# Performance work log

Hardware: AMD Instinct MI355X
Metric: run time of the kernel (lower is better)

## Reference

```python
import jax, jax.numpy as jnp
import numpy as np

V, E, H, D = 32000, 512, 512, 512  # vocab, emb_dim, enc_hid_dim, dec_hid_dim
B, S, T = 32, 64, 48               # batch, src_len, trg_len


def _gru_cell(x, h, Wih, Whh, bih, bhh):
    # PyTorch GRU cell semantics (gate order r, z, n)
    gi = x @ Wih.T + bih
    gh = h @ Whh.T + bhh
    ir, iz, i_n = jnp.split(gi, 3, axis=-1)
    hr, hz, h_n = jnp.split(gh, 3, axis=-1)
    r = jax.nn.sigmoid(ir + hr)
    z = jax.nn.sigmoid(iz + hz)
    n = jnp.tanh(i_n + r * h_n)
    return (1.0 - z) * n + z * h


def setup_inputs() -> dict:
    key = jax.random.key(0)
    ks = jax.random.split(key, 21)
    f = lambda k, shp: jax.random.normal(k, shp, dtype=jnp.float32) * 0.05
    inp = {
        'src': jax.random.randint(ks[0], (B, S), 0, V),
        'trg': jax.random.randint(ks[1], (T, B), 0, V),
        'emb': f(ks[2], (V, E)),
        'encf_Wih': f(ks[3], (3 * H, E)), 'encf_Whh': f(ks[4], (3 * H, H)),
        'encf_bih': f(ks[5], (3 * H,)), 'encf_bhh': f(ks[6], (3 * H,)),
        'encb_Wih': f(ks[7], (3 * H, E)), 'encb_Whh': f(ks[8], (3 * H, H)),
        'encb_bih': f(ks[9], (3 * H,)), 'encb_bhh': f(ks[10], (3 * H,)),
        'fc_W': f(ks[11], (D, 2 * H)), 'fc_b': f(ks[12], (D,)),
        'attn_W': f(ks[13], (D, D + 2 * H)), 'attn_v': f(ks[14], (D,)),
        'dec_Wih': f(ks[15], (3 * D, E + 2 * H)), 'dec_Whh': f(ks[16], (3 * D, D)),
        'dec_bih': f(ks[17], (3 * D,)), 'dec_bhh': f(ks[18], (3 * D,)),
        'out_W': f(ks[19], (V, 2 * H + D + E)),
        'out_b': jnp.zeros((V,), dtype=jnp.float32),
    }
    return inp


def _forward(src, trg, emb, encf_Wih, encf_Whh, encf_bih, encf_bhh,
             encb_Wih, encb_Whh, encb_bih, encb_bhh, fc_W, fc_b,
             attn_W, attn_v, dec_Wih, dec_Whh, dec_bih, dec_bhh, out_W, out_b):
    x = emb[src]                       # [B,S,E]
    xT = jnp.swapaxes(x, 0, 1)         # [S,B,E]
    h0 = jnp.zeros((src.shape[0], encf_Whh.shape[1]), dtype=x.dtype)

    def stepf(h, xt):
        h2 = _gru_cell(xt, h, encf_Wih, encf_Whh, encf_bih, encf_bhh)
        return h2, h2

    def stepb(h, xt):
        h2 = _gru_cell(xt, h, encb_Wih, encb_Whh, encb_bih, encb_bhh)
        return h2, h2

    hf, yf = jax.lax.scan(stepf, h0, xT)
    hb, yb = jax.lax.scan(stepb, h0, xT[::-1])
    # [B,S,2H] bidirectional encoder outputs (backward stream re-reversed)
    enc_out = jnp.concatenate([jnp.swapaxes(yf, 0, 1), jnp.swapaxes(yb[::-1], 0, 1)], axis=-1)
    # decoder init state from final fwd/bwd hidden
    s0 = jnp.tanh(jnp.concatenate([hf, hb], axis=-1) @ fc_W.T + fc_b)  # [B,D]

    def dec_step(s, tok):
        e = emb[tok]  # [B,E]
        srep = jnp.broadcast_to(s[:, None, :], (s.shape[0], enc_out.shape[1], s.shape[1]))
        energy = jnp.tanh(jnp.concatenate([srep, enc_out], axis=-1) @ attn_W.T)  # [B,S,D]
        a = jax.nn.softmax(energy @ attn_v, axis=1)  # [B,S]
        c = jnp.einsum('bs,bsh->bh', a, enc_out)     # [B,2H]
        s2 = _gru_cell(jnp.concatenate([e, c], axis=-1), s, dec_Wih, dec_Whh, dec_bih, dec_bhh)
        pred = jnp.concatenate([s2, c, e], axis=-1) @ out_W.T + out_b  # [B,V]
        return s2, pred

    # teacher forcing: decoder inputs are trg[0..T-2]
    _, preds = jax.lax.scan(dec_step, s0, trg[:-1])
    out0 = jnp.zeros((1,) + preds.shape[1:], dtype=preds.dtype)  # outputs[0] stays zero
    return jnp.concatenate([out0, preds], axis=0)  # [T,B,V]


def reference(src, trg, emb, encf_Wih, encf_Whh, encf_bih, encf_bhh,
              encb_Wih, encb_Whh, encb_bih, encb_bhh, fc_W, fc_b,
              attn_W, attn_v, dec_Wih, dec_Whh, dec_bih, dec_bhh, out_W, out_b):
    return _forward(src, trg, emb, encf_Wih, encf_Whh, encf_bih, encf_bhh,
                    encb_Wih, encb_Whh, encb_bih, encb_bhh, fc_W, fc_b,
                    attn_W, attn_v, dec_Wih, dec_Whh, dec_bih, dec_bhh, out_W, out_b)
```

## Files before the change

kernel.cpp:

```cpp
#include <hip/hip_runtime.h>
#include <stdint.h>
#include <stddef.h>

typedef __attribute__((ext_vector_type(8))) short short8;
typedef __attribute__((ext_vector_type(4))) float f32x4;
typedef unsigned int u32;

__device__ inline unsigned short f2bf(float f) {
  union { float f; uint32_t u; } v; v.f = f;
  uint32_t u = v.u;
  u += 0x7FFFu + ((u >> 16) & 1u);
  return (unsigned short)(u >> 16);
}
__device__ inline float bf2f(unsigned short h) {
  union { uint32_t u; float f; } v; v.u = ((uint32_t)h) << 16; return v.f;
}
__device__ inline short8 pack8(float4 a, float4 b) {
  short8 r;
  r[0] = (short)f2bf(a.x); r[1] = (short)f2bf(a.y);
  r[2] = (short)f2bf(a.z); r[3] = (short)f2bf(a.w);
  r[4] = (short)f2bf(b.x); r[5] = (short)f2bf(b.y);
  r[6] = (short)f2bf(b.z); r[7] = (short)f2bf(b.w);
  return r;
}
__device__ inline float tanh_fast(float x) {
  float xc = fminf(fmaxf(x, -9.f), 9.f);
  float e = __expf(2.f * xc);
  return (e - 1.f) * __builtin_amdgcn_rcpf(e + 1.f);
}
__device__ inline float sigm_fast(float x) {
  float xc = fminf(fmaxf(x, -30.f), 30.f);
  return __builtin_amdgcn_rcpf(1.f + __expf(-xc));
}
__device__ inline void gl_lds16(const unsigned short* g, unsigned short* l) {
  __builtin_amdgcn_global_load_lds(
      (const __attribute__((address_space(1))) u32*)g,
      (__attribute__((address_space(3))) u32*)l, 16, 0, 0);
}

__global__ __launch_bounds__(128) void prep_gather(
    const int* __restrict__ src, const int* __restrict__ trg,
    const float* __restrict__ emb,
    unsigned short* __restrict__ xbf, unsigned short* __restrict__ ebf,
    unsigned short* __restrict__ Zbf) {
  int r = blockIdx.x, tid = threadIdx.x;
  if (r < 2048) {
    int b = r & 31, s = r >> 5;
    int tok = src[b * 64 + s];
    const float* e = emb + (size_t)tok * 512;
    float4 v = *(const float4*)(e + tid * 4);
    unsigned short* dst = xbf + (size_t)r * 512 + tid * 4;
    dst[0] = f2bf(v.x); dst[1] = f2bf(v.y); dst[2] = f2bf(v.z); dst[3] = f2bf(v.w);
  } else {
    int rr = r - 2048;
    int t = rr >> 5, b = rr & 31;
    unsigned short* dst = ebf + (size_t)rr * 512 + tid * 4;
    if (t < 47) {
      int tok = trg[t * 32 + b];
      const float* e = emb + (size_t)tok * 512;
      float4 v = *(const float4*)(e + tid * 4);
      unsigned short q0 = f2bf(v.x), q1 = f2bf(v.y), q2 = f2bf(v.z), q3 = f2bf(v.w);
      dst[0] = q0; dst[1] = q1; dst[2] = q2; dst[3] = q3;
      unsigned short* zd = Zbf + (size_t)rr * 2048 + 1536 + tid * 4;
      zd[0] = q0; zd[1] = q1; zd[2] = q2; zd[3] = q3;
    } else {
      dst[0] = 0; dst[1] = 0; dst[2] = 0; dst[3] = 0;
    }
  }
}

__global__ __launch_bounds__(64) void cvt_weights(
    const float* __restrict__ encfW, const float* __restrict__ encbW,
    const float* __restrict__ attnW, const float* __restrict__ decWhh,
    unsigned short* __restrict__ whFbf, unsigned short* __restrict__ whBbf,
    unsigned short* __restrict__ Wcat) {
  int r = blockIdx.x, c = threadIdx.x * 8;
  const float* s;
  unsigned short* d;
  if (r < 1536) { s = encfW + (size_t)r * 512 + c; d = whFbf + (size_t)r * 512 + c; }
  else if (r < 3072) { int q = r - 1536; s = encbW + (size_t)q * 512 + c; d = whBbf + (size_t)q * 512 + c; }
  else if (r < 3584) { int q = r - 3072; s = attnW + (size_t)q * 1536 + c; d = Wcat + (size_t)q * 512 + c; }
  else { int q = r - 3584; s = decWhh + (size_t)q * 512 + c; d = Wcat + (size_t)(q + 512) * 512 + c; }
  *(short8*)d = pack8(*(const float4*)s, *(const float4*)(s + 4));
}

template <bool ABF, bool BBF, bool WBF>
__global__ __launch_bounds__(256) void gemm_kernel(
    const void* __restrict__ Av, int lda,
    const void* __restrict__ Bv, int ldb, int bco,
    const float* __restrict__ bias,
    void* __restrict__ Cv, int ldc,
    int K, int Mvalid, int row_off) {
  __shared__ __align__(16) unsigned short As[128 * 32];
  __shared__ __align__(16) unsigned short Bs[128 * 32];
  const int tid = threadIdx.x;
  const int m0 = blockIdx.x * 128, n0 = blockIdx.y * 128;
  const int w = tid >> 6, lane = tid & 63;
  const int wm = w >> 1, wn = w & 1;
  const int fr = lane & 15, fq = lane >> 4;
  f32x4 acc[4][4];
#pragma unroll
  for (int mi = 0; mi < 4; ++mi)
#pragma unroll
    for (int ni = 0; ni < 4; ++ni) acc[mi][ni] = (f32x4){0.f, 0.f, 0.f, 0.f};
  for (int k0 = 0; k0 < K; k0 += 32) {
#pragma unroll
    for (int p = 0; p < 2; ++p) {
      int idx = p * 256 + tid;
      int row = idx >> 2, seg = idx & 3;
      if (ABF) {
        const unsigned short* Ab = (const unsigned short*)Av;
        *(short8*)(As + row * 32 + seg * 8) =
            *(const short8*)(Ab + (size_t)(m0 + row) * lda + k0 + seg * 8);
      } else {
        const float* Af = (const float*)Av;
        const float* ap = Af + (size_t)(m0 + row) * lda + k0 + seg * 8;
        *(short8*)(As + row * 32 + seg * 8) = pack8(*(const float4*)ap, *(const float4*)(ap + 4));
      }
      if (BBF) {
        const unsigned short* Bb = (const unsigned short*)Bv;
        *(short8*)(Bs + row * 32 + seg * 8) =
            *(const short8*)(Bb + (size_t)(n0 + row) * ldb + bco + k0 + seg * 8);
      } else {
        const float* Bf = (const float*)Bv;
        const float* bp = Bf + (size_t)(n0 + row) * ldb + bco + k0 + seg * 8;
        *(short8*)(Bs + row * 32 + seg * 8) = pack8(*(const float4*)bp, *(const float4*)(bp + 4));
      }
    }
    __syncthreads();
    short8 af[4], bfr[4];
#pragma unroll
    for (int mi = 0; mi < 4; ++mi)
      af[mi] = *(const short8*)(As + (wm * 64 + mi * 16 + fr) * 32 + fq * 8);
#pragma unroll
    for (int ni = 0; ni < 4; ++ni)
      bfr[ni] = *(const short8*)(Bs + (wn * 64 + ni * 16 + fr) * 32 + fq * 8);
#pragma unroll
    for (int mi = 0; mi < 4; ++mi)
#pragma unroll
      for (int ni = 0; ni < 4; ++ni)
        acc[mi][ni] = __builtin_amdgcn_mfma_f32_16x16x32_bf16(af[mi], bfr[ni], acc[mi][ni], 0, 0, 0);
    __syncthreads();
  }
#pragma unroll
  for (int mi = 0; mi < 4; ++mi)
#pragma unroll
    for (int ni = 0; ni < 4; ++ni) {
      int col = n0 + wn * 64 + ni * 16 + fr;
      float bv = bias ? bias[col] : 0.f;
#pragma unroll
      for (int j = 0; j < 4; ++j) {
        int rowm = m0 + wm * 64 + mi * 16 + fq * 4 + j;
        if (rowm < Mvalid) {
          float val = acc[mi][ni][j] + bv;
          if (WBF)
            ((unsigned short*)Cv)[(size_t)(rowm + row_off) * ldc + col] = f2bf(val);
          else
            ((float*)Cv)[(size_t)(rowm + row_off) * ldc + col] = val;
        }
      }
    }
}

__global__ __launch_bounds__(512, 1) void gemm_big8(
    const unsigned short* __restrict__ A,
    const unsigned short* __restrict__ B,
    const float* __restrict__ bias,
    float* __restrict__ C) {
  extern __shared__ char lds[];
  char* LA = lds;
  char* LB = lds + 65536;
  const int tid = threadIdx.x;
  const int w = tid >> 6, lane = tid & 63;
  int wg = blockIdx.x;
  {
    int x = wg & 7, i = wg >> 3;
    wg = (x < 6 ? x * 94 : 564 + (x - 6) * 93) + i;
  }
  const int m0 = (wg % 6) * 256, n0 = (wg / 6) * 256;
  const int wm = w >> 2, wn = w & 3;
  const int fr = lane & 15, fq = lane >> 4;

  auto stage = [&](const unsigned short* G, char* L, int rowbase, int kt, int h, int c) {
#pragma unroll
    for (int j = 0; j < 2; ++j) {
      int pbh = j * 8192 + w * 1024;
      int pl = pbh + lane * 16;
      int lb = pl ^ (((pl >> 7) & 7) << 4);
      int rl = lb >> 7, ch = (lb >> 4) & 7;
      gl_lds16(G + (size_t)(rowbase + h * 128 + rl) * 2048 + kt * 64 + ch * 8,
               (unsigned short*)(L + c * 32768 + h * 16384 + pbh));
    }
  };

  f32x4 acc[8][4];
#pragma unroll
  for (int mi = 0; mi < 8; ++mi)
#pragma unroll
    for (int ni = 0; ni < 4; ++ni) acc[mi][ni] = (f32x4){0.f, 0.f, 0.f, 0.f};

  stage(A, LA, m0, 0, 0, 0); stage(B, LB, n0, 0, 0, 0);
  stage(A, LA, m0, 0, 1, 0); stage(B, LB, n0, 0, 1, 0);
  asm volatile("s_waitcnt vmcnt(0)" ::: "memory");
  __builtin_amdgcn_s_barrier();

  short8 bfrag[8];
  for (int kt = 0; kt < 32; ++kt) {
    const int c = kt & 1;
    char* Abuf = LA + c * 32768;
    char* Bbuf = LB + c * 32768;
#pragma unroll
    for (int p = 0; p < 4; ++p) {
      if (kt < 31) {
        if (p == 0) {
          stage(A, LA, m0, kt + 1, 0, c ^ 1);
          stage(B, LB, n0, kt + 1, 0, c ^ 1);
        } else if (p == 1) {
          stage(A, LA, m0, kt + 1, 1, c ^ 1);
          stage(B, LB, n0, kt + 1, 1, c ^ 1);
        }
      }
      if (p == 0) {
#pragma unroll
        for (int ni = 0; ni < 4; ++ni)
#pragma unroll
          for (int ks = 0; ks < 2; ++ks) {
            int n = wn * 64 + ni * 16 + fr;
            int h = n >> 7, nl = n & 127;
            int lb = nl * 128 + ks * 64 + fq * 16;
            int pb = lb ^ (((lb >> 7) & 7) << 4);
            bfrag[ni * 2 + ks] = *(const short8*)(Bbuf + h * 16384 + pb);
          }
      }
      short8 afrag[4];
#pragma unroll
      for (int q = 0; q < 2; ++q)
#pragma unroll
        for (int ks = 0; ks < 2; ++ks) {
          int r = wm * 128 + (2 * p + q) * 16 + fr;
          int h = r >> 7, rl = r & 127;
          int lb = rl * 128 + ks * 64 + fq * 16;
          int pb = lb ^ (((lb >> 7) & 7) << 4);
          afrag[q * 2 + ks] = *(const short8*)(Abuf + h * 16384 + pb);
        }
      __builtin_amdgcn_s_setprio(1);
#pragma unroll
      for (int q = 0; q < 2; ++q)
#pragma unroll
        for (int ni = 0; ni < 4; ++ni)
#pragma unroll
          for (int ks = 0; ks < 2; ++ks)
            acc[2 * p + q][ni] = __builtin_amdgcn_mfma_f32_16x16x32_bf16(
                afrag[q * 2 + ks], bfrag[ni * 2 + ks], acc[2 * p + q][ni], 0, 0, 0);
      __builtin_amdgcn_s_setprio(0);
      if (p == 3) asm volatile("s_waitcnt vmcnt(0)" ::: "memory");
      __builtin_amdgcn_s_barrier();
    }
  }
#pragma unroll
  for (int mi = 0; mi < 8; ++mi)
#pragma unroll
    for (int ni = 0; ni < 4; ++ni) {
      int col = n0 + wn * 64 + ni * 16 + fr;
      float bv = bias[col];
#pragma unroll
      for (int j = 0; j < 4; ++j) {
        int row = m0 + wm * 128 + mi * 16 + fq * 4 + j;
        if (row < 1504) C[(size_t)(row + 32) * 32000 + col] = acc[mi][ni][j] + bv;
      }
    }
}

__global__ __launch_bounds__(512) void enc_step(
    const float* __restrict__ Gif, const float* __restrict__ Gib,
    const unsigned short* __restrict__ whFbf, const unsigned short* __restrict__ whBbf,
    const float* __restrict__ bhhF, const float* __restrict__ bhhB,
    unsigned short* __restrict__ hbf,
    float* __restrict__ hf32,
    unsigned short* __restrict__ ebo,
    float* __restrict__ hcat,
    const float* __restrict__ outW, unsigned short* __restrict__ outWbf, int nCvt,
    int t) {
  const int blk = blockIdx.x, tid = threadIdx.x;
  if (blk >= 32) {
    if (blk - 32 < nCvt) {
      size_t base4 = ((size_t)t * nCvt + (blk - 32)) * 1280;
      for (int i = tid; i < 1280; i += 512) {
        float4 v = ((const float4*)outW)[base4 + i];
        unsigned short* d = outWbf + (base4 + i) * 4;
        d[0] = f2bf(v.x); d[1] = f2bf(v.y); d[2] = f2bf(v.z); d[3] = f2bf(v.w);
      }
    }
    return;
  }
  const int dir = blk >> 4, slice = blk & 15, D0 = slice * 32;
  const unsigned short* Wbf = dir ? whBbf : whFbf;
  const float* Gi = dir ? Gib : Gif;
  const float* bhh = dir ? bhhB : bhhF;
  __shared__ __align__(16) unsigned short hlds[32 * 520];
  __shared__ __align__(16) float gl[96 * 33];
  const unsigned short* hb = hbf + dir * 32768 + (t & 1) * 16384;
  for (int c = tid; c < 32 * 64; c += 512) {
    int r = c >> 6, seg = c & 63;
    *(short8*)(hlds + r * 520 + seg * 8) = *(const short8*)(hb + r * 512 + seg * 8);
  }
  __syncthreads();
  const int w = tid >> 6, lane = tid & 63, fr = lane & 15, fq = lane >> 4;
  if (w < 6) {
    int row = w * 16 + fr;
    int gr = (row >> 5) * 512 + D0 + (row & 31);
    const unsigned short* wrow = Wbf + (size_t)gr * 512;
    f32x4 acc0 = {0.f, 0.f, 0.f, 0.f}, acc1 = {0.f, 0.f, 0.f, 0.f};
#pragma unroll
    for (int k0 = 0; k0 < 512; k0 += 32) {
      short8 bq = *(const short8*)(wrow + k0 + fq * 8);
      short8 a0 = *(const short8*)(hlds + fr * 520 + k0 + fq * 8);
      short8 a1 = *(const short8*)(hlds + (16 + fr) * 520 + k0 + fq * 8);
      acc0 = __builtin_amdgcn_mfma_f32_16x16x32_bf16(a0, bq, acc0, 0, 0, 0);
      acc1 = __builtin_amdgcn_mfma_f32_16x16x32_bf16(a1, bq, acc1, 0, 0, 0);
    }
#pragma unroll
    for (int j = 0; j < 4; ++j) {
      gl[row * 33 + fq * 4 + j] = acc0[j];
      gl[row * 33 + 16 + fq * 4 + j] = acc1[j];
    }
  }
  __syncthreads();
  const int srow = dir ? 63 - t : t;
  unsigned short* hnb = hbf + dir * 32768 + ((t + 1) & 1) * 16384;
  const float* hcur = hf32 + dir * 32768 + (t & 1) * 16384;
  float* hnf = hf32 + dir * 32768 + ((t + 1) & 1) * 16384;
#pragma unroll
  for (int rep = 0; rep < 2; ++rep) {
    int idx = rep * 512 + tid, b = idx >> 5, dl = idx & 31, d = D0 + dl;
    float ar = gl[dl * 33 + b] + bhh[d];
    float az = gl[(32 + dl) * 33 + b] + bhh[512 + d];
    float an = gl[(64 + dl) * 33 + b] + bhh[1024 + d];
    const float* gi = Gi + ((size_t)srow * 32 + b) * 1536;
    float r = sigm_fast(gi[d] + ar);
    float z = sigm_fast(gi[512 + d] + az);
    float n = tanh_fast(gi[1024 + d] + r * an);
    float h2 = (1.f - z) * n + z * hcur[b * 512 + d];
    hnb[b * 512 + d] = f2bf(h2);
    hnf[b * 512 + d] = h2;
    ebo[((size_t)b * 64 + srow) * 1024 + (size_t)dir * 512 + d] = f2bf(h2);
    if (t == 63) hcat[(size_t)b * 1024 + (size_t)dir * 512 + d] = h2;
  }
}

__global__ __launch_bounds__(512) void tanh_s0(const float* __restrict__ s0raw,
                                               float* __restrict__ sf32,
                                               unsigned short* __restrict__ sbf) {
  int idx = blockIdx.x * 512 + threadIdx.x;
  float v = tanhf(s0raw[idx]);
  sf32[idx] = v;
  sbf[idx] = f2bf(v);
}

__global__ __launch_bounds__(512) void dec_proj(
    const unsigned short* __restrict__ Wcat, const float* __restrict__ decBhh,
    const unsigned short* __restrict__ sbf, float* __restrict__ gout, int t) {
  const int g = blockIdx.x, tid = threadIdx.x;
  __shared__ __align__(16) unsigned short slds[32 * 520];
  const unsigned short* sb = sbf + (t & 1) * 16384;
  for (int c = tid; c < 32 * 64; c += 512) {
    int r = c >> 6, seg = c & 63;
    *(short8*)(slds + r * 520 + seg * 8) = *(const short8*)(sb + r * 512 + seg * 8);
  }
  __syncthreads();
  const int w = tid >> 6, lane = tid & 63, fr = lane & 15, fq = lane >> 4;
  const int mt = w >> 2, nt = w & 3;
  int rc = g * 64 + nt * 16 + fr;
  const unsigned short* wrow = Wcat + (size_t)rc * 512;
  f32x4 acc = {0.f, 0.f, 0.f, 0.f};
#pragma unroll
  for (int k0 = 0; k0 < 512; k0 += 32) {
    short8 a = *(const short8*)(slds + (mt * 16 + fr) * 520 + k0 + fq * 8);
    short8 bq = *(const short8*)(wrow + k0 + fq * 8);
    acc = __builtin_amdgcn_mfma_f32_16x16x32_bf16(a, bq, acc, 0, 0, 0);
  }
  float bv = rc < 512 ? 0.f : decBhh[rc - 512];
#pragma unroll
  for (int j = 0; j < 4; ++j)
    gout[(size_t)(mt * 16 + fq * 4 + j) * 2048 + rc] = acc[j] + bv;
}

__global__ __launch_bounds__(512) void dec_attn(
    const float* __restrict__ attnV,
    const unsigned short* __restrict__ epf, const unsigned short* __restrict__ ebo,
    const unsigned short* __restrict__ EP2b, const float* __restrict__ Gie,
    const float* __restrict__ gout,
    unsigned short* __restrict__ sbf, float* __restrict__ sf32,
    unsigned short* __restrict__ Zbf, int t) {
  const int b = blockIdx.x, tid = threadIdx.x;
  __shared__ __align__(16) float gout_f[2048];
  __shared__ float raw[64], aaw[64];
  __shared__ float vlds[512];
  vlds[tid] = attnV[tid];
  *(float4*)(gout_f + tid * 4) = *(const float4*)(gout + (size_t)b * 2048 + tid * 4);
  __syncthreads();
  const int s_i = tid >> 3, l8 = tid & 7;
  {
    float part = 0.f;
    const float* gp = gout_f + l8 * 64;
    const unsigned short* ep = epf + ((size_t)b * 64 + s_i) * 512 + l8 * 64;
    const float* vv = vlds + l8 * 64;
#pragma unroll
    for (int jc = 0; jc < 8; ++jc) {
      short8 e8 = *(const short8*)(ep + jc * 8);
      float4 g0 = *(const float4*)(gp + jc * 8);
      float4 g1 = *(const float4*)(gp + jc * 8 + 4);
      float4 v0 = *(const float4*)(vv + jc * 8);
      float4 v1 = *(const float4*)(vv + jc * 8 + 4);
      part += tanh_fast(g0.x + bf2f((unsigned short)e8[0])) * v0.x;
      part += tanh_fast(g0.y + bf2f((unsigned short)e8[1])) * v0.y;
      part += tanh_fast(g0.z + bf2f((unsigned short)e8[2])) * v0.z;
      part += tanh_fast(g0.w + bf2f((unsigned short)e8[3])) * v0.w;
      part += tanh_fast(g1.x + bf2f((unsigned short)e8[4])) * v1.x;
      part += tanh_fast(g1.y + bf2f((unsigned short)e8[5])) * v1.y;
      part += tanh_fast(g1.z + bf2f((unsigned short)e8[6])) * v1.z;
      part += tanh_fast(g1.w + bf2f((unsigned short)e8[7])) * v1.w;
    }
    part += __shfl_xor(part, 1);
    part += __shfl_xor(part, 2);
    part += __shfl_xor(part, 4);
    if (l8 == 0) raw[s_i] = part;
  }
  __syncthreads();
  if (tid < 64) {
    float x = raw[tid];
    float m = x;
#pragma unroll
    for (int k = 1; k < 64; k <<= 1) m = fmaxf(m, __shfl_xor(m, k));
    float e = __expf(x - m);
    float s = e;
#pragma unroll
    for (int k = 1; k < 64; k <<= 1) s += __shfl_xor(s, k);
    aaw[tid] = e * __builtin_amdgcn_rcpf(s);
  }
  __syncthreads();
  float c0 = 0.f, c1 = 0.f, g0a = 0.f, g1a = 0.f, g2a = 0.f;
  {
    const unsigned short* eb = ebo + (size_t)b * 64 * 1024 + tid;
    const unsigned short* e2 = EP2b + (size_t)b * 64 * 1536 + tid;
#pragma unroll 8
    for (int s2 = 0; s2 < 64; ++s2) {
      float a = aaw[s2];
      c0 += a * bf2f(eb[(size_t)s2 * 1024]);
      c1 += a * bf2f(eb[(size_t)s2 * 1024 + 512]);
      g0a += a * bf2f(e2[(size_t)s2 * 1536]);
      g1a += a * bf2f(e2[(size_t)s2 * 1536 + 512]);
      g2a += a * bf2f(e2[(size_t)s2 * 1536 + 1024]);
    }
  }
  const float* gie = Gie + ((size_t)t * 32 + b) * 1536;
  float sprev = sf32[(t & 1) * 16384 + b * 512 + tid];
  float rr = sigm_fast(gie[tid] + g0a + gout_f[512 + tid]);
  float zz = sigm_fast(gie[512 + tid] + g1a + gout_f[1024 + tid]);
  float nn = tanh_fast(gie[1024 + tid] + g2a + rr * gout_f[1536 + tid]);
  float s2v = (1.f - zz) * nn + zz * sprev;
  sbf[((t + 1) & 1) * 16384 + b * 512 + tid] = f2bf(s2v);
  sf32[((t + 1) & 1) * 16384 + b * 512 + tid] = s2v;
  size_t zrow = ((size_t)t * 32 + b) * 2048;
  Zbf[zrow + tid] = f2bf(s2v);
  Zbf[zrow + 512 + tid] = f2bf(c0);
  Zbf[zrow + 1024 + tid] = f2bf(c1);
}

extern "C" void kernel_launch(void* const* d_in, const int* in_sizes, int n_in,
                              void* d_out, int out_size, void* d_ws, size_t ws_size,
                              hipStream_t stream) {
  (void)in_sizes; (void)n_in; (void)out_size;
  const int* src = (const int*)d_in[0];
  const int* trg = (const int*)d_in[1];
  const float* emb = (const float*)d_in[2];
  const float* encf_Wih = (const float*)d_in[3];
  const float* encf_Whh = (const float*)d_in[4];
  const float* encf_bih = (const float*)d_in[5];
  const float* encf_bhh = (const float*)d_in[6];
  const float* encb_Wih = (const float*)d_in[7];
  const float* encb_Whh = (const float*)d_in[8];
  const float* encb_bih = (const float*)d_in[9];
  const float* encb_bhh = (const float*)d_in[10];
  const float* fc_W = (const float*)d_in[11];
  const float* fc_b = (const float*)d_in[12];
  const float* attn_W = (const float*)d_in[13];
  const float* attn_v = (const float*)d_in[14];
  const float* dec_Wih = (const float*)d_in[15];
  const float* dec_Whh = (const float*)d_in[16];
  const float* dec_bih = (const float*)d_in[17];
  const float* dec_bhh = (const float*)d_in[18];
  const float* out_W = (const float*)d_in[19];
  const float* out_b = (const float*)d_in[20];
  float* out = (float*)d_out;

  char* p = (char*)d_ws;
  size_t off = 0;
  auto alloc = [&](size_t bytes) {
    void* r = p + off;
    off = (off + bytes + 255) & ~(size_t)255;
    return r;
  };
  unsigned short* xbf = (unsigned short*)alloc((size_t)2048 * 512 * 2);
  unsigned short* ebf = (unsigned short*)alloc((size_t)1536 * 512 * 2);
  unsigned short* Zbf = (unsigned short*)alloc((size_t)1536 * 2048 * 2);
  float* Gif = (float*)alloc((size_t)2048 * 1536 * 4);
  float* Gib = (float*)alloc((size_t)2048 * 1536 * 4);
  float* Gie = (float*)alloc((size_t)1536 * 1536 * 4);
  unsigned short* ebo = (unsigned short*)alloc((size_t)2048 * 1024 * 2);
  unsigned short* epf = (unsigned short*)alloc((size_t)2048 * 512 * 2);
  unsigned short* EP2b = (unsigned short*)alloc((size_t)2048 * 1536 * 2);
  unsigned short* whFbf = (unsigned short*)alloc((size_t)1536 * 512 * 2);
  unsigned short* whBbf = (unsigned short*)alloc((size_t)1536 * 512 * 2);
  unsigned short* Wcat = (unsigned short*)alloc((size_t)2048 * 512 * 2);
  unsigned short* hbf = (unsigned short*)alloc((size_t)2 * 2 * 32 * 512 * 2);
  float* hf32 = (float*)alloc((size_t)2 * 2 * 32 * 512 * 4);
  float* hcat = (float*)alloc((size_t)32 * 1024 * 4);
  float* s0raw = (float*)alloc((size_t)32 * 512 * 4);
  unsigned short* sbf = (unsigned short*)alloc((size_t)2 * 32 * 512 * 2);
  float* sf32 = (float*)alloc((size_t)2 * 32 * 512 * 4);
  float* gout = (float*)alloc((size_t)32 * 2048 * 4);
  unsigned short* outWbf = (unsigned short*)alloc((size_t)32000 * 2048 * 2);
  const bool bigB = (off <= ws_size);

  hipMemsetAsync(hbf, 0, (size_t)2 * 2 * 32 * 512 * 2, stream);
  hipMemsetAsync(hf32, 0, (size_t)2 * 2 * 32 * 512 * 4, stream);
  hipMemsetAsync(d_out, 0, (size_t)32 * 32000 * 4, stream);

  prep_gather<<<3584, 128, 0, stream>>>(src, trg, emb, xbf, ebf, Zbf);
  cvt_weights<<<5120, 64, 0, stream>>>(encf_Whh, encb_Whh, attn_W, dec_Whh,
                                       whFbf, whBbf, Wcat);

  gemm_kernel<true, false, false><<<dim3(16, 12), 256, 0, stream>>>(
      xbf, 512, encf_Wih, 512, 0, encf_bih, Gif, 1536, 512, 2048, 0);
  gemm_kernel<true, false, false><<<dim3(16, 12), 256, 0, stream>>>(
      xbf, 512, encb_Wih, 512, 0, encb_bih, Gib, 1536, 512, 2048, 0);
  gemm_kernel<true, false, false><<<dim3(12, 12), 256, 0, stream>>>(
      ebf, 512, dec_Wih, 1536, 0, dec_bih, Gie, 1536, 512, 1536, 0);

  const int nCvt = bigB ? 200 : 0;
  for (int t = 0; t < 64; ++t)
    enc_step<<<32 + nCvt, 512, 0, stream>>>(Gif, Gib, whFbf, whBbf, encf_bhh, encb_bhh,
                                            hbf, hf32, ebo, hcat, out_W, outWbf, nCvt, t);

  gemm_kernel<false, false, false><<<dim3(1, 4), 256, 0, stream>>>(
      hcat, 1024, fc_W, 1024, 0, fc_b, s0raw, 512, 1024, 32, 0);
  tanh_s0<<<32, 512, 0, stream>>>(s0raw, sf32, sbf);

  gemm_kernel<true, false, true><<<dim3(16, 4), 256, 0, stream>>>(
      ebo, 1024, attn_W, 1536, 512, nullptr, epf, 512, 1024, 2048, 0);
  gemm_kernel<true, false, true><<<dim3(16, 12), 256, 0, stream>>>(
      ebo, 1024, dec_Wih, 1536, 512, nullptr, EP2b, 1536, 1024, 2048, 0);

  for (int t = 0; t < 47; ++t) {
    dec_proj<<<32, 512, 0, stream>>>(Wcat, dec_bhh, sbf, gout, t);
    dec_attn<<<32, 512, 0, stream>>>(attn_v, epf, ebo, EP2b, Gie, gout,
                                     sbf, sf32, Zbf, t);
  }

  if (bigB) {
    hipFuncSetAttribute((const void*)gemm_big8,
                        hipFuncAttributeMaxDynamicSharedMemorySize, 131072);
    gemm_big8<<<750, 512, 131072, stream>>>(Zbf, outWbf, out_b, out);
  } else {
    gemm_kernel<true, false, false><<<dim3(12, 250), 256, 0, stream>>>(
        Zbf, 2048, out_W, 2048, 0, out_b, out, 32000, 2048, 1504, 32);
  }
}
```

Before: 1.872 ms.

## Replace per-timestep encoder and decoder launches with persistent kernels using flag-based grid sync

The 64 per-step encoder launches and the 94 decoder launches (proj and attn) become two persistent kernels. Blocks exchange hidden state through global buffers written with atomic exchanges and signal completion with per-step flags that other blocks poll. Hidden state is kept in registers across steps, and the output-weight conversion runs as a grid-stride loop on the extra blocks alongside the encoder. The aim is to remove kernel launch overhead and the implicit global barriers between steps. In exchange it relies on all blocks being co-resident, adds spin-wait latency, and the polling loop has a bounded timeout.

```diff
diff --git a/kernel.cpp b/kernel.cpp
--- a/kernel.cpp
+++ b/kernel.cpp
@@ -5,6 +5,7 @@
 typedef __attribute__((ext_vector_type(8))) short short8;
 typedef __attribute__((ext_vector_type(4))) float f32x4;
 typedef unsigned int u32;
+typedef unsigned long long u64;
 
 __device__ inline unsigned short f2bf(float f) {
   union { float f; uint32_t u; } v; v.f = f;
@@ -31,6 +32,34 @@
 __device__ inline float sigm_fast(float x) {
   float xc = fminf(fmaxf(x, -30.f), 30.f);
   return __builtin_amdgcn_rcpf(1.f + __expf(-xc));
+}
+__device__ inline u64 pack2f(float a, float b) {
+  return (u64)__float_as_uint(a) | ((u64)__float_as_uint(b) << 32);
+}
+__device__ inline void st_x64(u64* p, u64 v) {
+  u64 old = __hip_atomic_exchange(p, v, __ATOMIC_RELAXED, __HIP_MEMORY_SCOPE_AGENT);
+  asm volatile("" :: "v"(old));
+}
+__device__ inline u64 ld_x64(u64* p) {
+  return __hip_atomic_fetch_add(p, 0ULL, __ATOMIC_RELAXED, __HIP_MEMORY_SCOPE_AGENT);
+}
+__device__ inline void st_flag(int* f) {
+  int old = __hip_atomic_exchange(f, 1, __ATOMIC_RELAXED, __HIP_MEMORY_SCOPE_AGENT);
+  asm volatile("" :: "v"(old));
+}
+__device__ inline int ld_flag(int* f) {
+  return __hip_atomic_fetch_add(f, 0, __ATOMIC_RELAXED, __HIP_MEMORY_SCOPE_AGENT);
+}
+__device__ inline void poll_flags(int* base, int n, int tid) {
+  if (tid < 64) {
+    bool done = tid >= n;
+    for (int it = 0; it < (1 << 17); ++it) {
+      if (!done) done = ld_flag(base + tid) != 0;
+      if (__all((int)done)) break;
+      __builtin_amdgcn_s_sleep(2);
+    }
+  }
+  __syncthreads();
 }
 __device__ inline void gl_lds16(const unsigned short* g, unsigned short* l) {
   __builtin_amdgcn_global_load_lds(
@@ -271,25 +300,23 @@
     }
 }
 
-__global__ __launch_bounds__(512) void enc_step(
+__global__ __launch_bounds__(512, 1) void enc_all(
     const float* __restrict__ Gif, const float* __restrict__ Gib,
     const unsigned short* __restrict__ whFbf, const unsigned short* __restrict__ whBbf,
     const float* __restrict__ bhhF, const float* __restrict__ bhhB,
-    unsigned short* __restrict__ hbf,
-    float* __restrict__ hf32,
+    u64* hmb,
     unsigned short* __restrict__ ebo,
     float* __restrict__ hcat,
-    const float* __restrict__ outW, unsigned short* __restrict__ outWbf, int nCvt,
-    int t) {
+    const float* __restrict__ outW, unsigned short* __restrict__ outWbf,
+    long long nCvt4, int* hflag) {
   const int blk = blockIdx.x, tid = threadIdx.x;
   if (blk >= 32) {
-    if (blk - 32 < nCvt) {
-      size_t base4 = ((size_t)t * nCvt + (blk - 32)) * 1280;
-      for (int i = tid; i < 1280; i += 512) {
-        float4 v = ((const float4*)outW)[base4 + i];
-        unsigned short* d = outWbf + (base4 + i) * 4;
-        d[0] = f2bf(v.x); d[1] = f2bf(v.y); d[2] = f2bf(v.z); d[3] = f2bf(v.w);
-      }
+    long long i = (long long)(blk - 32) * 512 + tid;
+    long long stride = (long long)(gridDim.x - 32) * 512;
+    for (; i < nCvt4; i += stride) {
+      float4 v = ((const float4*)outW)[i];
+      unsigned short* d = outWbf + i * 4;
+      d[0] = f2bf(v.x); d[1] = f2bf(v.y); d[2] = f2bf(v.z); d[3] = f2bf(v.w);
     }
     return;
   }
@@ -299,52 +326,78 @@
   const float* bhh = dir ? bhhB : bhhF;
   __shared__ __align__(16) unsigned short hlds[32 * 520];
   __shared__ __align__(16) float gl[96 * 33];
-  const unsigned short* hb = hbf + dir * 32768 + (t & 1) * 16384;
-  for (int c = tid; c < 32 * 64; c += 512) {
-    int r = c >> 6, seg = c & 63;
-    *(short8*)(hlds + r * 520 + seg * 8) = *(const short8*)(hb + r * 512 + seg * 8);
-  }
-  __syncthreads();
+  __shared__ __align__(16) unsigned short pub[32 * 32];
+  u64* hb = hmb + (size_t)dir * 8192;
+  int* mf = hflag + dir * 1024;
   const int w = tid >> 6, lane = tid & 63, fr = lane & 15, fq = lane >> 4;
-  if (w < 6) {
-    int row = w * 16 + fr;
-    int gr = (row >> 5) * 512 + D0 + (row & 31);
-    const unsigned short* wrow = Wbf + (size_t)gr * 512;
-    f32x4 acc0 = {0.f, 0.f, 0.f, 0.f}, acc1 = {0.f, 0.f, 0.f, 0.f};
-#pragma unroll
-    for (int k0 = 0; k0 < 512; k0 += 32) {
-      short8 bq = *(const short8*)(wrow + k0 + fq * 8);
-      short8 a0 = *(const short8*)(hlds + fr * 520 + k0 + fq * 8);
-      short8 a1 = *(const short8*)(hlds + (16 + fr) * 520 + k0 + fq * 8);
-      acc0 = __builtin_amdgcn_mfma_f32_16x16x32_bf16(a0, bq, acc0, 0, 0, 0);
-      acc1 = __builtin_amdgcn_mfma_f32_16x16x32_bf16(a1, bq, acc1, 0, 0, 0);
-    }
-#pragma unroll
-    for (int j = 0; j < 4; ++j) {
-      gl[row * 33 + fq * 4 + j] = acc0[j];
-      gl[row * 33 + 16 + fq * 4 + j] = acc1[j];
-    }
-  }
-  __syncthreads();
-  const int srow = dir ? 63 - t : t;
-  unsigned short* hnb = hbf + dir * 32768 + ((t + 1) & 1) * 16384;
-  const float* hcur = hf32 + dir * 32768 + (t & 1) * 16384;
-  float* hnf = hf32 + dir * 32768 + ((t + 1) & 1) * 16384;
-#pragma unroll
-  for (int rep = 0; rep < 2; ++rep) {
-    int idx = rep * 512 + tid, b = idx >> 5, dl = idx & 31, d = D0 + dl;
-    float ar = gl[dl * 33 + b] + bhh[d];
-    float az = gl[(32 + dl) * 33 + b] + bhh[512 + d];
-    float an = gl[(64 + dl) * 33 + b] + bhh[1024 + d];
-    const float* gi = Gi + ((size_t)srow * 32 + b) * 1536;
-    float r = sigm_fast(gi[d] + ar);
-    float z = sigm_fast(gi[512 + d] + az);
-    float n = tanh_fast(gi[1024 + d] + r * an);
-    float h2 = (1.f - z) * n + z * hcur[b * 512 + d];
-    hnb[b * 512 + d] = f2bf(h2);
-    hnf[b * 512 + d] = h2;
-    ebo[((size_t)b * 64 + srow) * 1024 + (size_t)dir * 512 + d] = f2bf(h2);
-    if (t == 63) hcat[(size_t)b * 1024 + (size_t)dir * 512 + d] = h2;
+  float hprev[2] = {0.f, 0.f};
+  for (int t = 0; t < 64; ++t) {
+    {
+      u64* hs = hb + (t & 1) * 4096;
+      u64 t0 = ld_x64(hs + tid), t1 = ld_x64(hs + tid + 512);
+      u64 t2 = ld_x64(hs + tid + 1024), t3 = ld_x64(hs + tid + 1536);
+      u64 t4 = ld_x64(hs + tid + 2048), t5 = ld_x64(hs + tid + 2560);
+      u64 t6 = ld_x64(hs + tid + 3072), t7 = ld_x64(hs + tid + 3584);
+      int i0 = tid;
+      *(u64*)(hlds + ((i0) >> 7) * 520 + ((i0) & 127) * 4) = t0;
+      *(u64*)(hlds + ((i0 + 512) >> 7) * 520 + ((i0 + 512) & 127) * 4) = t1;
+      *(u64*)(hlds + ((i0 + 1024) >> 7) * 520 + ((i0 + 1024) & 127) * 4) = t2;
+      *(u64*)(hlds + ((i0 + 1536) >> 7) * 520 + ((i0 + 1536) & 127) * 4) = t3;
+      *(u64*)(hlds + ((i0 + 2048) >> 7) * 520 + ((i0 + 2048) & 127) * 4) = t4;
+      *(u64*)(hlds + ((i0 + 2560) >> 7) * 520 + ((i0 + 2560) & 127) * 4) = t5;
+      *(u64*)(hlds + ((i0 + 3072) >> 7) * 520 + ((i0 + 3072) & 127) * 4) = t6;
+      *(u64*)(hlds + ((i0 + 3584) >> 7) * 520 + ((i0 + 3584) & 127) * 4) = t7;
+    }
+    __syncthreads();
+    if (w < 6) {
+      int row = w * 16 + fr;
+      int gr = (row >> 5) * 512 + D0 + (row & 31);
+      const unsigned short* wrow = Wbf + (size_t)gr * 512;
+      f32x4 acc0 = {0.f, 0.f, 0.f, 0.f}, acc1 = {0.f, 0.f, 0.f, 0.f};
+#pragma unroll
+      for (int k0 = 0; k0 < 512; k0 += 32) {
+        short8 bq = *(const short8*)(wrow + k0 + fq * 8);
+        short8 a0 = *(const short8*)(hlds + fr * 520 + k0 + fq * 8);
+        short8 a1 = *(const short8*)(hlds + (16 + fr) * 520 + k0 + fq * 8);
+        acc0 = __builtin_amdgcn_mfma_f32_16x16x32_bf16(a0, bq, acc0, 0, 0, 0);
+        acc1 = __builtin_amdgcn_mfma_f32_16x16x32_bf16(a1, bq, acc1, 0, 0, 0);
+      }
+#pragma unroll
+      for (int j = 0; j < 4; ++j) {
+        gl[row * 33 + fq * 4 + j] = acc0[j];
+        gl[row * 33 + 16 + fq * 4 + j] = acc1[j];
+      }
+    }
+    __syncthreads();
+    const int srow = dir ? 63 - t : t;
+#pragma unroll
+    for (int rep = 0; rep < 2; ++rep) {
+      int idx = rep * 512 + tid, b = idx >> 5, dl = idx & 31, d = D0 + dl;
+      float ar = gl[dl * 33 + b] + bhh[d];
+      float az = gl[(32 + dl) * 33 + b] + bhh[512 + d];
+      float an = gl[(64 + dl) * 33 + b] + bhh[1024 + d];
+      const float* gi = Gi + ((size_t)srow * 32 + b) * 1536;
+      float r = sigm_fast(gi[d] + ar);
+      float z = sigm_fast(gi[512 + d] + az);
+      float n = tanh_fast(gi[1024 + d] + r * an);
+      float h2 = (1.f - z) * n + z * hprev[rep];
+      hprev[rep] = h2;
+      pub[b * 32 + dl] = f2bf(h2);
+      ebo[((size_t)b * 64 + srow) * 1024 + (size_t)dir * 512 + d] = f2bf(h2);
+      if (t == 63) hcat[(size_t)b * 1024 + (size_t)dir * 512 + d] = h2;
+    }
+    __syncthreads();
+    if (t < 63) {
+      if (tid < 256) {
+        int b = tid >> 3, c4 = tid & 7;
+        st_x64(hb + ((t + 1) & 1) * 4096 + b * 128 + (D0 >> 2) + c4,
+               *(const u64*)(pub + b * 32 + c4 * 4));
+      }
+      asm volatile("s_waitcnt vmcnt(0)" ::: "memory");
+      __syncthreads();
+      if (tid == 0) st_flag(&mf[t * 16 + slice]);
+      poll_flags(&mf[t * 16], 16, tid);
+    }
   }
 }
 
@@ -357,114 +410,159 @@
   sbf[idx] = f2bf(v);
 }
 
-__global__ __launch_bounds__(512) void dec_proj(
+__global__ __launch_bounds__(512, 1) void dec_all(
     const unsigned short* __restrict__ Wcat, const float* __restrict__ decBhh,
-    const unsigned short* __restrict__ sbf, float* __restrict__ gout, int t) {
-  const int g = blockIdx.x, tid = threadIdx.x;
-  __shared__ __align__(16) unsigned short slds[32 * 520];
-  const unsigned short* sb = sbf + (t & 1) * 16384;
-  for (int c = tid; c < 32 * 64; c += 512) {
-    int r = c >> 6, seg = c & 63;
-    *(short8*)(slds + r * 520 + seg * 8) = *(const short8*)(sb + r * 512 + seg * 8);
-  }
-  __syncthreads();
-  const int w = tid >> 6, lane = tid & 63, fr = lane & 15, fq = lane >> 4;
-  const int mt = w >> 2, nt = w & 3;
-  int rc = g * 64 + nt * 16 + fr;
-  const unsigned short* wrow = Wcat + (size_t)rc * 512;
-  f32x4 acc = {0.f, 0.f, 0.f, 0.f};
-#pragma unroll
-  for (int k0 = 0; k0 < 512; k0 += 32) {
-    short8 a = *(const short8*)(slds + (mt * 16 + fr) * 520 + k0 + fq * 8);
-    short8 bq = *(const short8*)(wrow + k0 + fq * 8);
-    acc = __builtin_amdgcn_mfma_f32_16x16x32_bf16(a, bq, acc, 0, 0, 0);
-  }
-  float bv = rc < 512 ? 0.f : decBhh[rc - 512];
-#pragma unroll
-  for (int j = 0; j < 4; ++j)
-    gout[(size_t)(mt * 16 + fq * 4 + j) * 2048 + rc] = acc[j] + bv;
-}
-
-__global__ __launch_bounds__(512) void dec_attn(
     const float* __restrict__ attnV,
+    u64* smb, const float* __restrict__ s0f,
     const unsigned short* __restrict__ epf, const unsigned short* __restrict__ ebo,
     const unsigned short* __restrict__ EP2b, const float* __restrict__ Gie,
-    const float* __restrict__ gout,
-    unsigned short* __restrict__ sbf, float* __restrict__ sf32,
-    unsigned short* __restrict__ Zbf, int t) {
-  const int b = blockIdx.x, tid = threadIdx.x;
-  __shared__ __align__(16) float gout_f[2048];
-  __shared__ float raw[64], aaw[64];
-  __shared__ float vlds[512];
-  vlds[tid] = attnV[tid];
-  *(float4*)(gout_f + tid * 4) = *(const float4*)(gout + (size_t)b * 2048 + tid * 4);
-  __syncthreads();
-  const int s_i = tid >> 3, l8 = tid & 7;
-  {
-    float part = 0.f;
-    const float* gp = gout_f + l8 * 64;
-    const unsigned short* ep = epf + ((size_t)b * 64 + s_i) * 512 + l8 * 64;
-    const float* vv = vlds + l8 * 64;
-#pragma unroll
-    for (int jc = 0; jc < 8; ++jc) {
-      short8 e8 = *(const short8*)(ep + jc * 8);
-      float4 g0 = *(const float4*)(gp + jc * 8);
-      float4 g1 = *(const float4*)(gp + jc * 8 + 4);
-      float4 v0 = *(const float4*)(vv + jc * 8);
-      float4 v1 = *(const float4*)(vv + jc * 8 + 4);
-      part += tanh_fast(g0.x + bf2f((unsigned short)e8[0])) * v0.x;
-      part += tanh_fast(g0.y + bf2f((unsigned short)e8[1])) * v0.y;
-      part += tanh_fast(g0.z + bf2f((unsigned short)e8[2])) * v0.z;
-      part += tanh_fast(g0.w + bf2f((unsigned short)e8[3])) * v0.w;
-      part += tanh_fast(g1.x + bf2f((unsigned short)e8[4])) * v1.x;
-      part += tanh_fast(g1.y + bf2f((unsigned short)e8[5])) * v1.y;
-      part += tanh_fast(g1.z + bf2f((unsigned short)e8[6])) * v1.z;
-      part += tanh_fast(g1.w + bf2f((unsigned short)e8[7])) * v1.w;
-    }
-    part += __shfl_xor(part, 1);
-    part += __shfl_xor(part, 2);
-    part += __shfl_xor(part, 4);
-    if (l8 == 0) raw[s_i] = part;
-  }
-  __syncthreads();
-  if (tid < 64) {
-    float x = raw[tid];
-    float m = x;
-#pragma unroll
-    for (int k = 1; k < 64; k <<= 1) m = fmaxf(m, __shfl_xor(m, k));
-    float e = __expf(x - m);
-    float s = e;
-#pragma unroll
-    for (int k = 1; k < 64; k <<= 1) s += __shfl_xor(s, k);
-    aaw[tid] = e * __builtin_amdgcn_rcpf(s);
-  }
-  __syncthreads();
-  float c0 = 0.f, c1 = 0.f, g0a = 0.f, g1a = 0.f, g2a = 0.f;
-  {
-    const unsigned short* eb = ebo + (size_t)b * 64 * 1024 + tid;
-    const unsigned short* e2 = EP2b + (size_t)b * 64 * 1536 + tid;
+    u64* gout64, unsigned short* __restrict__ Zbf,
+    int* gflag, int* sflag) {
+  __shared__ __align__(16) char smem[43008];
+  const int blk = blockIdx.x, tid = threadIdx.x;
+  if (blk < 32) {
+    const int g = blk;
+    unsigned short* slds = (unsigned short*)smem;
+    float* glds = (float*)(smem + 33280);
+    const int w = tid >> 6, lane = tid & 63, fr = lane & 15, fq = lane >> 4;
+    const int mt = w >> 2, nt = w & 3;
+    const int rc = g * 64 + nt * 16 + fr;
+    const unsigned short* wrow = Wcat + (size_t)rc * 512;
+    const float bv = rc < 512 ? 0.f : decBhh[rc - 512];
+    for (int t = 0; t < 47; ++t) {
+      if (t > 0) poll_flags(&sflag[(t - 1) * 32], 32, tid);
+      {
+        u64* ss = smb + (t & 1) * 4096;
+        u64 t0 = ld_x64(ss + tid), t1 = ld_x64(ss + tid + 512);
+        u64 t2 = ld_x64(ss + tid + 1024), t3 = ld_x64(ss + tid + 1536);
+        u64 t4 = ld_x64(ss + tid + 2048), t5 = ld_x64(ss + tid + 2560);
+        u64 t6 = ld_x64(ss + tid + 3072), t7 = ld_x64(ss + tid + 3584);
+        int i0 = tid;
+        *(u64*)(slds + ((i0) >> 7) * 520 + ((i0) & 127) * 4) = t0;
+        *(u64*)(slds + ((i0 + 512) >> 7) * 520 + ((i0 + 512) & 127) * 4) = t1;
+        *(u64*)(slds + ((i0 + 1024) >> 7) * 520 + ((i0 + 1024) & 127) * 4) = t2;
+        *(u64*)(slds + ((i0 + 1536) >> 7) * 520 + ((i0 + 1536) & 127) * 4) = t3;
+        *(u64*)(slds + ((i0 + 2048) >> 7) * 520 + ((i0 + 2048) & 127) * 4) = t4;
+        *(u64*)(slds + ((i0 + 2560) >> 7) * 520 + ((i0 + 2560) & 127) * 4) = t5;
+        *(u64*)(slds + ((i0 + 3072) >> 7) * 520 + ((i0 + 3072) & 127) * 4) = t6;
+        *(u64*)(slds + ((i0 + 3584) >> 7) * 520 + ((i0 + 3584) & 127) * 4) = t7;
+      }
+      __syncthreads();
+      {
+        f32x4 acc = {0.f, 0.f, 0.f, 0.f};
+#pragma unroll
+        for (int k0 = 0; k0 < 512; k0 += 32) {
+          short8 a = *(const short8*)(slds + (mt * 16 + fr) * 520 + k0 + fq * 8);
+          short8 bq = *(const short8*)(wrow + k0 + fq * 8);
+          acc = __builtin_amdgcn_mfma_f32_16x16x32_bf16(a, bq, acc, 0, 0, 0);
+        }
+#pragma unroll
+        for (int j = 0; j < 4; ++j)
+          glds[(mt * 16 + fq * 4 + j) * 68 + nt * 16 + fr] = acc[j] + bv;
+      }
+      __syncthreads();
+      {
+        int b = tid >> 4, q = tid & 15;
+        const float* gp = glds + b * 68 + q * 4;
+        st_x64(gout64 + b * 1024 + g * 32 + q * 2, pack2f(gp[0], gp[1]));
+        st_x64(gout64 + b * 1024 + g * 32 + q * 2 + 1, pack2f(gp[2], gp[3]));
+      }
+      asm volatile("s_waitcnt vmcnt(0)" ::: "memory");
+      __syncthreads();
+      if (tid == 0) st_flag(&gflag[t * 32 + g]);
+    }
+  } else {
+    const int b = blk - 32;
+    float* gout_f = (float*)smem;
+    unsigned short* sout = (unsigned short*)(smem + 8192);
+    float* raw = (float*)(smem + 9216);
+    float* aaw = (float*)(smem + 9472);
+    float* vlds = (float*)(smem + 9728);
+    vlds[tid] = attnV[tid];
+    const int s_i = tid >> 3, l8 = tid & 7;
+    float sreg = s0f[b * 512 + tid];
+    __syncthreads();
+    for (int t = 0; t < 47; ++t) {
+      poll_flags(&gflag[t * 32], 32, tid);
+      {
+        u64 v0 = ld_x64(gout64 + b * 1024 + tid * 2);
+        u64 v1 = ld_x64(gout64 + b * 1024 + tid * 2 + 1);
+        ((u64*)gout_f)[tid * 2] = v0;
+        ((u64*)gout_f)[tid * 2 + 1] = v1;
+      }
+      __syncthreads();
+      {
+        float part = 0.f;
+        const float* gp = gout_f + l8 * 64;
+        const unsigned short* ep = epf + ((size_t)b * 64 + s_i) * 512 + l8 * 64;
+        const float* vv = vlds + l8 * 64;
+#pragma unroll
+        for (int jc = 0; jc < 8; ++jc) {
+          short8 e8 = *(const short8*)(ep + jc * 8);
+          float4 g0 = *(const float4*)(gp + jc * 8);
+          float4 g1 = *(const float4*)(gp + jc * 8 + 4);
+          float4 v0 = *(const float4*)(vv + jc * 8);
+          float4 v1 = *(const float4*)(vv + jc * 8 + 4);
+          part += tanh_fast(g0.x + bf2f((unsigned short)e8[0])) * v0.x;
+          part += tanh_fast(g0.y + bf2f((unsigned short)e8[1])) * v0.y;
+          part += tanh_fast(g0.z + bf2f((unsigned short)e8[2])) * v0.z;
+          part += tanh_fast(g0.w + bf2f((unsigned short)e8[3])) * v0.w;
+          part += tanh_fast(g1.x + bf2f((unsigned short)e8[4])) * v1.x;
+          part += tanh_fast(g1.y + bf2f((unsigned short)e8[5])) * v1.y;
+          part += tanh_fast(g1.z + bf2f((unsigned short)e8[6])) * v1.z;
+          part += tanh_fast(g1.w + bf2f((unsigned short)e8[7])) * v1.w;
+        }
+        part += __shfl_xor(part, 1);
+        part += __shfl_xor(part, 2);
+        part += __shfl_xor(part, 4);
+        if (l8 == 0) raw[s_i] = part;
+      }
+      __syncthreads();
+      if (tid < 64) {
+        float x = raw[tid];
+        float m = x;
+#pragma unroll
+        for (int k = 1; k < 64; k <<= 1) m = fmaxf(m, __shfl_xor(m, k));
+        float e = __expf(x - m);
+        float s = e;
+#pragma unroll
+        for (int k = 1; k < 64; k <<= 1) s += __shfl_xor(s, k);
+        aaw[tid] = e * __builtin_amdgcn_rcpf(s);
+      }
+      __syncthreads();
+      float c0 = 0.f, c1 = 0.f, g0a = 0.f, g1a = 0.f, g2a = 0.f;
+      {
+        const unsigned short* eb = ebo + (size_t)b * 64 * 1024 + tid;
+        const unsigned short* e2 = EP2b + (size_t)b * 64 * 1536 + tid;
 #pragma unroll 8
-    for (int s2 = 0; s2 < 64; ++s2) {
-      float a = aaw[s2];
-      c0 += a * bf2f(eb[(size_t)s2 * 1024]);
-      c1 += a * bf2f(eb[(size_t)s2 * 1024 + 512]);
-      g0a += a * bf2f(e2[(size_t)s2 * 1536]);
-      g1a += a * bf2f(e2[(size_t)s2 * 1536 + 512]);
-      g2a += a * bf2f(e2[(size_t)s2 * 1536 + 1024]);
-    }
-  }
-  const float* gie = Gie + ((size_t)t * 32 + b) * 1536;
-  float sprev = sf32[(t & 1) * 16384 + b * 512 + tid];
-  float rr = sigm_fast(gie[tid] + g0a + gout_f[512 + tid]);
-  float zz = sigm_fast(gie[512 + tid] + g1a + gout_f[1024 + tid]);
-  float nn = tanh_fast(gie[1024 + tid] + g2a + rr * gout_f[1536 + tid]);
-  float s2v = (1.f - zz) * nn + zz * sprev;
-  sbf[((t + 1) & 1) * 16384 + b * 512 + tid] = f2bf(s2v);
-  sf32[((t + 1) & 1) * 16384 + b * 512 + tid] = s2v;
-  size_t zrow = ((size_t)t * 32 + b) * 2048;
-  Zbf[zrow + tid] = f2bf(s2v);
-  Zbf[zrow + 512 + tid] = f2bf(c0);
-  Zbf[zrow + 1024 + tid] = f2bf(c1);
+        for (int s2 = 0; s2 < 64; ++s2) {
+          float a = aaw[s2];
+          c0 += a * bf2f(eb[(size_t)s2 * 1024]);
+          c1 += a * bf2f(eb[(size_t)s2 * 1024 + 512]);
+          g0a += a * bf2f(e2[(size_t)s2 * 1536]);
+          g1a += a * bf2f(e2[(size_t)s2 * 1536 + 512]);
+          g2a += a * bf2f(e2[(size_t)s2 * 1536 + 1024]);
+        }
+      }
+      const float* gie = Gie + ((size_t)t * 32 + b) * 1536;
+      float rr = sigm_fast(gie[tid] + g0a + gout_f[512 + tid]);
+      float zz = sigm_fast(gie[512 + tid] + g1a + gout_f[1024 + tid]);
+      float nn = tanh_fast(gie[1024 + tid] + g2a + rr * gout_f[1536 + tid]);
+      float s2v = (1.f - zz) * nn + zz * sreg;
+      sreg = s2v;
+      sout[tid] = f2bf(s2v);
+      __syncthreads();
+      if (tid < 128)
+        st_x64(smb + ((t + 1) & 1) * 4096 + b * 128 + tid, *(const u64*)(sout + tid * 4));
+      asm volatile("s_waitcnt vmcnt(0)" ::: "memory");
+      __syncthreads();
+      if (tid == 0) st_flag(&sflag[t * 32 + b]);
+      size_t zrow = ((size_t)t * 32 + b) * 2048;
+      Zbf[zrow + tid] = f2bf(s2v);
+      Zbf[zrow + 512 + tid] = f2bf(c0);
+      Zbf[zrow + 1024 + tid] = f2bf(c1);
+    }
+  }
 }
 
 extern "C" void kernel_launch(void* const* d_in, const int* in_sizes, int n_in,
@@ -501,6 +599,11 @@
     off = (off + bytes + 255) & ~(size_t)255;
     return r;
   };
+  const int NFLG = 47 * 32 * 2 + 2048;
+  int* flg = (int*)alloc(NFLG * 4);
+  int* gflag = flg;
+  int* sflag = flg + 47 * 32;
+  int* hflag = flg + 47 * 32 * 2;
   unsigned short* xbf = (unsigned short*)alloc((size_t)2048 * 512 * 2);
   unsigned short* ebf = (unsigned short*)alloc((size_t)1536 * 512 * 2);
   unsigned short* Zbf = (unsigned short*)alloc((size_t)1536 * 2048 * 2);
@@ -513,18 +616,17 @@
   unsigned short* whFbf = (unsigned short*)alloc((size_t)1536 * 512 * 2);
   unsigned short* whBbf = (unsigned short*)alloc((size_t)1536 * 512 * 2);
   unsigned short* Wcat = (unsigned short*)alloc((size_t)2048 * 512 * 2);
-  unsigned short* hbf = (unsigned short*)alloc((size_t)2 * 2 * 32 * 512 * 2);
-  float* hf32 = (float*)alloc((size_t)2 * 2 * 32 * 512 * 4);
+  u64* hmb = (u64*)alloc((size_t)2 * 2 * 4096 * 8);
   float* hcat = (float*)alloc((size_t)32 * 1024 * 4);
   float* s0raw = (float*)alloc((size_t)32 * 512 * 4);
-  unsigned short* sbf = (unsigned short*)alloc((size_t)2 * 32 * 512 * 2);
-  float* sf32 = (float*)alloc((size_t)2 * 32 * 512 * 4);
-  float* gout = (float*)alloc((size_t)32 * 2048 * 4);
+  float* s0f = (float*)alloc((size_t)32 * 512 * 4);
+  u64* smb = (u64*)alloc((size_t)2 * 4096 * 8);
+  u64* gout64 = (u64*)alloc((size_t)32 * 1024 * 8);
   unsigned short* outWbf = (unsigned short*)alloc((size_t)32000 * 2048 * 2);
   const bool bigB = (off <= ws_size);
 
-  hipMemsetAsync(hbf, 0, (size_t)2 * 2 * 32 * 512 * 2, stream);
-  hipMemsetAsync(hf32, 0, (size_t)2 * 2 * 32 * 512 * 4, stream);
+  hipMemsetAsync(flg, 0, NFLG * 4, stream);
+  hipMemsetAsync(hmb, 0, (size_t)2 * 2 * 4096 * 8, stream);
   hipMemsetAsync(d_out, 0, (size_t)32 * 32000 * 4, stream);
 
   prep_gather<<<3584, 128, 0, stream>>>(src, trg, emb, xbf, ebf, Zbf);
@@ -538,25 +640,22 @@
   gemm_kernel<true, false, false><<<dim3(12, 12), 256, 0, stream>>>(
       ebf, 512, dec_Wih, 1536, 0, dec_bih, Gie, 1536, 512, 1536, 0);
 
-  const int nCvt = bigB ? 200 : 0;
-  for (int t = 0; t < 64; ++t)
-    enc_step<<<32 + nCvt, 512, 0, stream>>>(Gif, Gib, whFbf, whBbf, encf_bhh, encb_bhh,
-                                            hbf, hf32, ebo, hcat, out_W, outWbf, nCvt, t);
+  const int nCvtBlocks = bigB ? 200 : 0;
+  enc_all<<<32 + nCvtBlocks, 512, 0, stream>>>(
+      Gif, Gib, whFbf, whBbf, encf_bhh, encb_bhh, hmb, ebo, hcat,
+      out_W, outWbf, bigB ? (long long)32000 * 2048 / 4 : 0, hflag);
 
   gemm_kernel<false, false, false><<<dim3(1, 4), 256, 0, stream>>>(
       hcat, 1024, fc_W, 1024, 0, fc_b, s0raw, 512, 1024, 32, 0);
-  tanh_s0<<<32, 512, 0, stream>>>(s0raw, sf32, sbf);
+  tanh_s0<<<32, 512, 0, stream>>>(s0raw, s0f, (unsigned short*)smb);
 
   gemm_kernel<true, false, true><<<dim3(16, 4), 256, 0, stream>>>(
       ebo, 1024, attn_W, 1536, 512, nullptr, epf, 512, 1024, 2048, 0);
   gemm_kernel<true, false, true><<<dim3(16, 12), 256, 0, stream>>>(
       ebo, 1024, dec_Wih, 1536, 512, nullptr, EP2b, 1536, 1024, 2048, 0);
 
-  for (int t = 0; t < 47; ++t) {
-    dec_proj<<<32, 512, 0, stream>>>(Wcat, dec_bhh, sbf, gout, t);
-    dec_attn<<<32, 512, 0, stream>>>(attn_v, epf, ebo, EP2b, Gie, gout,
-                                     sbf, sf32, Zbf, t);
-  }
+  dec_all<<<64, 512, 0, stream>>>(Wcat, dec_bhh, attn_v, smb, s0f,
+                                  epf, ebo, EP2b, Gie, gout64, Zbf, gflag, sflag);
 
   if (bigB) {
     hipFuncSetAttribute((const void*)gemm_big8,
```

New measurement: 2.419 ms. 1.29x slower.
